# Performance work log

Measured on AMD Instinct MI355X. Metric: run time of the kernel, lower is better.

Reference implementation:

```python
import jax, jax.numpy as jnp
import numpy as np

N_NODES = 100000
N_EDGES = 1200000
D = 64


def setup_inputs() -> dict:
    key = jax.random.key(0)
    ks = jax.random.split(key, 11)
    feats = jax.random.normal(ks[0], (N_NODES, D), dtype=jnp.float32)
    src = jax.random.randint(ks[1], (N_EDGES,), 0, N_NODES)
    dst = jax.random.randint(ks[2], (N_EDGES,), 0, N_NODES)
    s = 0.1  # small init scale
    W1 = jax.random.normal(ks[3], (D, D), dtype=jnp.float32) * s
    b1 = jnp.zeros((D,), dtype=jnp.float32)
    Wr1 = jax.random.normal(ks[4], (D, D), dtype=jnp.float32) * s
    br1 = jnp.zeros((D,), dtype=jnp.float32)
    W2 = jax.random.normal(ks[5], (D, D), dtype=jnp.float32) * s
    b2 = jnp.zeros((D,), dtype=jnp.float32)
    Wr2 = jax.random.normal(ks[6], (D, D), dtype=jnp.float32) * s
    br2 = jnp.zeros((D,), dtype=jnp.float32)
    return {"feats": feats, "W1": W1, "b1": b1, "Wr1": Wr1, "br1": br1,
            "W2": W2, "b2": b2, "Wr2": Wr2, "br2": br2,
            "src": src, "dst": dst}


def _gcn_layer(x, W, b, Wr, br, src, dst):
    # dgl GraphConv(norm='none'): aggregate sum of transformed neighbor feats + bias, then ReLU
    xw = x @ W                                        # [N, D]
    agg = jax.ops.segment_sum(xw[src], dst, num_segments=x.shape[0])  # gather-scatter
    conv = jax.nn.relu(agg + b)
    # residual branch: activation(Linear(feats))
    res = jax.nn.relu(x @ Wr + br)
    return conv + res  # dropout=0.0, batchnorm=False


def reference(feats, W1, b1, Wr1, br1, W2, b2, Wr2, br2, src, dst):
    h = _gcn_layer(feats, W1, b1, Wr1, br1, src, dst)
    h = _gcn_layer(h, W2, b2, Wr2, br2, src, dst)
    return h
```

## Files before the change

### kernel.cpp

```cpp
#include <hip/hip_runtime.h>

#define D 64
#define NBMAX 256
#define BCHUNK 4096
#define CAP 8192

typedef unsigned short ushort_t;
typedef __attribute__((ext_vector_type(8))) short bf16x8;
typedef __attribute__((ext_vector_type(4))) float floatx4;

static __device__ __forceinline__ ushort_t f2bf(float x) {
  unsigned u = __float_as_uint(x);
  unsigned r = (u + 0x7FFF + ((u >> 16) & 1)) >> 16;
  return (ushort_t)r;
}
static __device__ __forceinline__ float bf2f(ushort_t u) {
  return __uint_as_float(((unsigned)u) << 16);
}

__global__ __launch_bounds__(256) void gemm_res_mfma_kernel(
    const float* __restrict__ x, const float* __restrict__ W,
    const float* __restrict__ Wr, const float* __restrict__ br,
    ushort_t* __restrict__ xw, ushort_t* __restrict__ res, int n_nodes) {
  const int lane = threadIdx.x & 63;
  const int wid = threadIdx.x >> 6;
  const int sub = lane & 15;
  const int q = lane >> 4;

  bf16x8 bW[4][2], bR[4][2];
#pragma unroll
  for (int t = 0; t < 4; ++t) {
#pragma unroll
    for (int s = 0; s < 2; ++s) {
      bf16x8 fw, fr;
#pragma unroll
      for (int j = 0; j < 8; ++j) {
        const int k = s * 32 + q * 8 + j;
        const int c = t * 16 + sub;
        fw[j] = (short)f2bf(W[k * D + c]);
        fr[j] = (short)f2bf(Wr[k * D + c]);
      }
      bW[t][s] = fw;
      bR[t][s] = fr;
    }
  }
  float brv[4];
#pragma unroll
  for (int t = 0; t < 4; ++t) brv[t] = br[t * 16 + sub];

  const int n_tiles = (n_nodes + 15) >> 4;
  const int wave_id = blockIdx.x * 4 + wid;
  const int n_waves = gridDim.x * 4;
  for (int tile = wave_id; tile < n_tiles; tile += n_waves) {
    const int n0 = tile << 4;
    const bool full = (n0 + 16 <= n_nodes);
    bf16x8 a0h, a0l, a1h, a1l;
    float v[16];
    if (full) {
      const float* xp = x + (size_t)(n0 + sub) * D + q * 8;
      *(float4*)(v + 0)  = *(const float4*)(xp);
      *(float4*)(v + 4)  = *(const float4*)(xp + 4);
      *(float4*)(v + 8)  = *(const float4*)(xp + 32);
      *(float4*)(v + 12) = *(const float4*)(xp + 36);
    } else {
      const bool ok = (n0 + sub) < n_nodes;
      const float* xp = x + (size_t)(n0 + sub) * D + q * 8;
#pragma unroll
      for (int j = 0; j < 8; ++j) {
        v[j] = ok ? xp[j] : 0.f;
        v[8 + j] = ok ? xp[32 + j] : 0.f;
      }
    }
#pragma unroll
    for (int j = 0; j < 8; ++j) {
      const ushort_t h0 = f2bf(v[j]);
      a0h[j] = (short)h0;
      a0l[j] = (short)f2bf(v[j] - bf2f(h0));
      const ushort_t h1 = f2bf(v[8 + j]);
      a1h[j] = (short)h1;
      a1l[j] = (short)f2bf(v[8 + j] - bf2f(h1));
    }
    floatx4 accW[4], accR[4];
#pragma unroll
    for (int t = 0; t < 4; ++t) {
      accW[t] = (floatx4){0.f, 0.f, 0.f, 0.f};
      accR[t] = (floatx4){0.f, 0.f, 0.f, 0.f};
    }
#pragma unroll
    for (int t = 0; t < 4; ++t) {
      accW[t] = __builtin_amdgcn_mfma_f32_16x16x32_bf16(a0h, bW[t][0], accW[t], 0, 0, 0);
      accW[t] = __builtin_amdgcn_mfma_f32_16x16x32_bf16(a0l, bW[t][0], accW[t], 0, 0, 0);
      accW[t] = __builtin_amdgcn_mfma_f32_16x16x32_bf16(a1h, bW[t][1], accW[t], 0, 0, 0);
      accW[t] = __builtin_amdgcn_mfma_f32_16x16x32_bf16(a1l, bW[t][1], accW[t], 0, 0, 0);
      accR[t] = __builtin_amdgcn_mfma_f32_16x16x32_bf16(a0h, bR[t][0], accR[t], 0, 0, 0);
      accR[t] = __builtin_amdgcn_mfma_f32_16x16x32_bf16(a0l, bR[t][0], accR[t], 0, 0, 0);
      accR[t] = __builtin_amdgcn_mfma_f32_16x16x32_bf16(a1h, bR[t][1], accR[t], 0, 0, 0);
      accR[t] = __builtin_amdgcn_mfma_f32_16x16x32_bf16(a1l, bR[t][1], accR[t], 0, 0, 0);
    }
    if (full) {
#pragma unroll
      for (int t = 0; t < 4; ++t) {
#pragma unroll
        for (int i = 0; i < 4; ++i) {
          const size_t r = (size_t)(n0 + q * 4 + i) * D + t * 16 + sub;
          xw[r] = f2bf(accW[t][i]);
          res[r] = f2bf(fmaxf(accR[t][i] + brv[t], 0.f));
        }
      }
    } else {
#pragma unroll
      for (int t = 0; t < 4; ++t) {
#pragma unroll
        for (int i = 0; i < 4; ++i) {
          const int rr = n0 + q * 4 + i;
          if (rr < n_nodes) {
            const size_t r = (size_t)rr * D + t * 16 + sub;
            xw[r] = f2bf(accW[t][i]);
            res[r] = f2bf(fmaxf(accR[t][i] + brv[t], 0.f));
          }
        }
      }
    }
  }
}


__global__ __launch_bounds__(256) void bucket_count_kernel(
    const int* __restrict__ dst, int* __restrict__ counts, int n_edges) {
  __shared__ int hloc[NBMAX];
  const int t = threadIdx.x;
  hloc[t] = 0;
  __syncthreads();
  const int n4 = n_edges >> 2;
  const int stride = gridDim.x * blockDim.x;
  const int4* dst4 = (const int4*)dst;
  for (int i = blockIdx.x * blockDim.x + t; i < n4; i += stride) {
    const int4 d = dst4[i];
    atomicAdd(&hloc[d.x >> 9], 1);
    atomicAdd(&hloc[d.y >> 9], 1);
    atomicAdd(&hloc[d.z >> 9], 1);
    atomicAdd(&hloc[d.w >> 9], 1);
  }
  if (blockIdx.x == 0 && t == 0) {
    for (int e = n4 << 2; e < n_edges; ++e) atomicAdd(&counts[dst[e] >> 9], 1);
  }
  __syncthreads();
  atomicAdd(&counts[t], hloc[t]);
}

__global__ __launch_bounds__(256) void scan_buckets_kernel(
    const int* __restrict__ counts, int* __restrict__ bucket_base,
    int* __restrict__ gtail, int nbuckets, int* __restrict__ off_tail,
    int n_edges) {
  __shared__ int sc[NBMAX];
  const int t = threadIdx.x;
  const int c = (t < nbuckets) ? counts[t] : 0;
  sc[t] = c;
  __syncthreads();
  for (int off = 1; off < NBMAX; off <<= 1) {
    const int v = (t >= off) ? sc[t - off] : 0;
    __syncthreads();
    sc[t] += v;
    __syncthreads();
  }
  const int excl = sc[t] - c;
  if (t < nbuckets) {
    bucket_base[t] = excl;
    gtail[t] = excl;
  }
  if (t == nbuckets) bucket_base[t] = excl;
  if (t == 0) *off_tail = n_edges;
}

__global__ __launch_bounds__(256) void binpack_kernel(
    const int* __restrict__ src, const int* __restrict__ dst,
    int* __restrict__ gtail, unsigned* __restrict__ packed, int n_edges) {
  __shared__ int hist[NBMAX], start[NBMAX], cur[NBMAX], gpos[NBMAX];
  __shared__ unsigned sorted[BCHUNK];
  __shared__ unsigned char bktid[BCHUNK];
  const int t = threadIdx.x;
  const int nchunk = (n_edges + BCHUNK - 1) / BCHUNK;
  for (int c = blockIdx.x; c < nchunk; c += gridDim.x) {
    cur[t] = 0;
    __syncthreads();
    const int e0 = c * BCHUNK;
    const int m = min(BCHUNK, n_edges - e0);
    int bk[16];
    unsigned pk[16];
#pragma unroll
    for (int k = 0; k < 16; ++k) {
      const int e = e0 + k * 256 + t;
      if (e < n_edges) {
        const int d = dst[e];
        const int s = src[e];
        bk[k] = d >> 9;
        pk[k] = ((unsigned)(d & 511) << 23) | (unsigned)s;
        atomicAdd(&cur[bk[k]], 1);
      } else {
        bk[k] = -1;
      }
    }
    __syncthreads();
    const int h = cur[t];
    hist[t] = h;
    start[t] = h;
    __syncthreads();
    for (int off = 1; off < NBMAX; off <<= 1) {
      const int v = (t >= off) ? start[t - off] : 0;
      __syncthreads();
      start[t] += v;
      __syncthreads();
    }
    const int excl = start[t] - h;
    __syncthreads();
    start[t] = excl;
    cur[t] = excl;
    __syncthreads();
#pragma unroll
    for (int k = 0; k < 16; ++k) {
      if (bk[k] >= 0) {
        const int pos = atomicAdd(&cur[bk[k]], 1);
        sorted[pos] = pk[k];
        bktid[pos] = (unsigned char)bk[k];
      }
    }
    __syncthreads();
    if (h > 0) gpos[t] = atomicAdd(&gtail[t], h);
    __syncthreads();
    for (int j = t; j < m; j += 256) {
      const int b = bktid[j];
      packed[gpos[b] + j - start[b]] = sorted[j];
    }
    __syncthreads();
  }
}

__global__ __launch_bounds__(256) void bucket_csr_kernel(
    const unsigned* __restrict__ packed, const int* __restrict__ bucket_base,
    int* __restrict__ csr_off, int* __restrict__ csr_src, int n_nodes) {
  __shared__ int sc[2][512];
  __shared__ int cur[512];
  __shared__ unsigned outbuf[CAP];
  const int b = blockIdx.x;
  const int t = threadIdx.x;
  const int n0 = b << 9;
  const int nn = min(512, n_nodes - n0);
  const int base = bucket_base[b];
  const int cntE = bucket_base[b + 1] - base;
  cur[t] = 0;
  cur[t + 256] = 0;
  __syncthreads();
  for (int i = base + t; i < base + cntE; i += 256)
    atomicAdd(&cur[packed[i] >> 23], 1);
  __syncthreads();
  const int h0 = cur[t];
  const int h1 = cur[t + 256];
  sc[0][t] = h0;
  sc[0][t + 256] = h1;
  __syncthreads();
  int pin = 0;
  for (int off = 1; off < 512; off <<= 1) {
    sc[1 - pin][t] = sc[pin][t] + ((t >= off) ? sc[pin][t - off] : 0);
    sc[1 - pin][t + 256] =
        sc[pin][t + 256] + ((t + 256 >= off) ? sc[pin][t + 256 - off] : 0);
    __syncthreads();
    pin ^= 1;
  }
  const int excl0 = sc[pin][t] - h0;
  const int excl1 = sc[pin][t + 256] - h1;
  if (t < nn) csr_off[n0 + t] = base + excl0;
  if (t + 256 < nn) csr_off[n0 + t + 256] = base + excl1;
  cur[t] = excl0;
  cur[t + 256] = excl1;
  __syncthreads();
  if (cntE <= CAP) {
    for (int i = base + t; i < base + cntE; i += 256) {
      const unsigned u = packed[i];
      const int pos = atomicAdd(&cur[u >> 23], 1);
      outbuf[pos] = u & 0x7FFFFFu;
    }
    __syncthreads();
    for (int j = t; j < cntE; j += 256) csr_src[base + j] = (int)outbuf[j];
  } else {
    for (int i = base + t; i < base + cntE; i += 256) {
      const unsigned u = packed[i];
      const int pos = atomicAdd(&cur[u >> 23], 1);
      csr_src[base + pos] = (int)(u & 0x7FFFFFu);
    }
  }
}

__global__ __launch_bounds__(256) void gather_combine_kernel(
    const ushort_t* __restrict__ xw, const ushort_t* __restrict__ res,
    const float* __restrict__ b, const int* __restrict__ csr_off,
    const int* __restrict__ csr_src, float* __restrict__ out, int n_nodes) {
  const int lane = threadIdx.x & 63;
  const int wid = threadIdx.x >> 6;
  const int grp = lane >> 4;
  const int sub = lane & 15;
  const float4 bvec = *(const float4*)(b + sub * 4);
  const int n_tiles = (n_nodes + 3) >> 2;
  for (int tile = blockIdx.x; tile < n_tiles; tile += gridDim.x) {
    const int n = tile * 4 + wid;
    if (n >= n_nodes) continue;
    const int e0 = csr_off[n];
    const int e1 = csr_off[n + 1];
    float4 acc = make_float4(0.f, 0.f, 0.f, 0.f);
    for (int base_e = e0; base_e < e1; base_e += 64) {
      const int m = min(64, e1 - base_e);
      const int idxv = (base_e + lane < e1) ? csr_src[base_e + lane] : 0;
      for (int j = 0; j < m; j += 4) {
        const int idx = __shfl(idxv, j + grp, 64);
        if (j + grp < m) {
          const ushort4 v =
              *(const ushort4*)(xw + ((size_t)idx << 6) + (sub << 2));
          acc.x += bf2f(v.x);
          acc.y += bf2f(v.y);
          acc.z += bf2f(v.z);
          acc.w += bf2f(v.w);
        }
      }
    }
#pragma unroll
    for (int mask = 32; mask >= 16; mask >>= 1) {
      acc.x += __shfl_xor(acc.x, mask, 64);
      acc.y += __shfl_xor(acc.y, mask, 64);
      acc.z += __shfl_xor(acc.z, mask, 64);
      acc.w += __shfl_xor(acc.w, mask, 64);
    }
    if (grp == 0) {
      const ushort4 r =
          *(const ushort4*)(res + ((size_t)n << 6) + (sub << 2));
      float4 o;
      o.x = fmaxf(acc.x + bvec.x, 0.f) + bf2f(r.x);
      o.y = fmaxf(acc.y + bvec.y, 0.f) + bf2f(r.y);
      o.z = fmaxf(acc.z + bvec.z, 0.f) + bf2f(r.z);
      o.w = fmaxf(acc.w + bvec.w, 0.f) + bf2f(r.w);
      *(float4*)(out + ((size_t)n << 6) + (sub << 2)) = o;
    }
  }
}

extern "C" void kernel_launch(void* const* d_in, const int* in_sizes, int n_in,
                              void* d_out, int out_size, void* d_ws, size_t ws_size,
                              hipStream_t stream) {
  const float* feats = (const float*)d_in[0];
  const float* W1  = (const float*)d_in[1];
  const float* b1  = (const float*)d_in[2];
  const float* Wr1 = (const float*)d_in[3];
  const float* br1 = (const float*)d_in[4];
  const float* W2  = (const float*)d_in[5];
  const float* b2  = (const float*)d_in[6];
  const float* Wr2 = (const float*)d_in[7];
  const float* br2 = (const float*)d_in[8];
  const int* src = (const int*)d_in[9];
  const int* dst = (const int*)d_in[10];
  const int n_nodes = in_sizes[0] / D;
  const int n_edges = in_sizes[9];
  float* out = (float*)d_out;

  const int nbuckets = (n_nodes + 511) >> 9;

  ushort_t* xw = (ushort_t*)d_ws;
  ushort_t* res = xw + (size_t)n_nodes * D;
  int* csr_off = (int*)(res + (size_t)n_nodes * D);
  int* csr_src = csr_off + (n_nodes + 1);
  int* counts = csr_src + n_edges;
  int* bucket_base = counts + NBMAX;
  int* gtail = bucket_base + NBMAX + 1;
  unsigned* packed = (unsigned*)xw;

  const int tiles = (n_nodes + 3) / 4;
  const int gblocks = tiles < 2048 ? tiles : 2048;
  const int cblocks = (n_edges / 4 + 255) / 256 < 1024 ? (n_edges / 4 + 255) / 256 : 1024;
  const int nchunk = (n_edges + BCHUNK - 1) / BCHUNK;
  const int pblocks = nchunk < 1024 ? nchunk : 1024;
  const int mblocks = 1024;
  dim3 blk(256);

  hipMemsetAsync(counts, 0, NBMAX * sizeof(int), stream);
  bucket_count_kernel<<<cblocks, blk, 0, stream>>>(dst, counts, n_edges);
  scan_buckets_kernel<<<1, NBMAX, 0, stream>>>(counts, bucket_base, gtail,
                                               nbuckets, csr_off + n_nodes,
                                               n_edges);
  binpack_kernel<<<pblocks, blk, 0, stream>>>(src, dst, gtail, packed, n_edges);
  bucket_csr_kernel<<<nbuckets, blk, 0, stream>>>(packed, bucket_base, csr_off,
                                                  csr_src, n_nodes);

  gemm_res_mfma_kernel<<<mblocks, blk, 0, stream>>>(feats, W1, Wr1, br1, xw, res, n_nodes);
  gather_combine_kernel<<<gblocks, blk, 0, stream>>>(
      xw, res, b1, csr_off, csr_src, out, n_nodes);

  gemm_res_mfma_kernel<<<mblocks, blk, 0, stream>>>(out, W2, Wr2, br2, xw, res, n_nodes);
  gather_combine_kernel<<<gblocks, blk, 0, stream>>>(
      xw, res, b2, csr_off, csr_src, out, n_nodes);
}
```

Measured before the change: 268.3 us.

## Drop bucket count pass with fixed-capacity buckets and fuse layer-1 gather with layer-2 GEMM

Removes the bucket_count and scan kernels plus the memset. Each bucket now gets a fixed-capacity slot (CAP_PACK) in the packed buffer, and bucket_csr recomputes bucket offsets from the final tails. The layer-1 gather/combine is fused with the layer-2 linear transforms through an LDS tile and split-bf16 MFMA, so the fp32 intermediate never goes to global memory. The first GEMM also initializes the bucket tails. This cuts launches and a full pass over dst, but it assumes no bucket exceeds 12288 edges and that the caller supplies a larger workspace.

```diff
diff --git a/kernel.cpp b/kernel.cpp
--- a/kernel.cpp
+++ b/kernel.cpp
@@ -4,6 +4,7 @@
 #define NBMAX 256
 #define BCHUNK 4096
 #define CAP 8192
+#define CAP_PACK 12288
 
 typedef unsigned short ushort_t;
 typedef __attribute__((ext_vector_type(8))) short bf16x8;
@@ -21,7 +22,12 @@
 __global__ __launch_bounds__(256) void gemm_res_mfma_kernel(
     const float* __restrict__ x, const float* __restrict__ W,
     const float* __restrict__ Wr, const float* __restrict__ br,
-    ushort_t* __restrict__ xw, ushort_t* __restrict__ res, int n_nodes) {
+    ushort_t* __restrict__ xw, ushort_t* __restrict__ res, int n_nodes,
+    int* __restrict__ gtail, int* __restrict__ off_tail, int n_edges) {
+  if (blockIdx.x == 0) {
+    if (threadIdx.x < NBMAX) gtail[threadIdx.x] = (int)threadIdx.x * CAP_PACK;
+    if (threadIdx.x == 0) *off_tail = n_edges;
+  }
   const int lane = threadIdx.x & 63;
   const int wid = threadIdx.x >> 6;
   const int sub = lane & 15;
@@ -124,58 +130,10 @@
   }
 }
 
-
-__global__ __launch_bounds__(256) void bucket_count_kernel(
-    const int* __restrict__ dst, int* __restrict__ counts, int n_edges) {
-  __shared__ int hloc[NBMAX];
-  const int t = threadIdx.x;
-  hloc[t] = 0;
-  __syncthreads();
-  const int n4 = n_edges >> 2;
-  const int stride = gridDim.x * blockDim.x;
-  const int4* dst4 = (const int4*)dst;
-  for (int i = blockIdx.x * blockDim.x + t; i < n4; i += stride) {
-    const int4 d = dst4[i];
-    atomicAdd(&hloc[d.x >> 9], 1);
-    atomicAdd(&hloc[d.y >> 9], 1);
-    atomicAdd(&hloc[d.z >> 9], 1);
-    atomicAdd(&hloc[d.w >> 9], 1);
-  }
-  if (blockIdx.x == 0 && t == 0) {
-    for (int e = n4 << 2; e < n_edges; ++e) atomicAdd(&counts[dst[e] >> 9], 1);
-  }
-  __syncthreads();
-  atomicAdd(&counts[t], hloc[t]);
-}
-
-__global__ __launch_bounds__(256) void scan_buckets_kernel(
-    const int* __restrict__ counts, int* __restrict__ bucket_base,
-    int* __restrict__ gtail, int nbuckets, int* __restrict__ off_tail,
-    int n_edges) {
-  __shared__ int sc[NBMAX];
-  const int t = threadIdx.x;
-  const int c = (t < nbuckets) ? counts[t] : 0;
-  sc[t] = c;
-  __syncthreads();
-  for (int off = 1; off < NBMAX; off <<= 1) {
-    const int v = (t >= off) ? sc[t - off] : 0;
-    __syncthreads();
-    sc[t] += v;
-    __syncthreads();
-  }
-  const int excl = sc[t] - c;
-  if (t < nbuckets) {
-    bucket_base[t] = excl;
-    gtail[t] = excl;
-  }
-  if (t == nbuckets) bucket_base[t] = excl;
-  if (t == 0) *off_tail = n_edges;
-}
-
 __global__ __launch_bounds__(256) void binpack_kernel(
     const int* __restrict__ src, const int* __restrict__ dst,
     int* __restrict__ gtail, unsigned* __restrict__ packed, int n_edges) {
-  __shared__ int hist[NBMAX], start[NBMAX], cur[NBMAX], gpos[NBMAX];
+  __shared__ int start[NBMAX], cur[NBMAX], gpos[NBMAX];
   __shared__ unsigned sorted[BCHUNK];
   __shared__ unsigned char bktid[BCHUNK];
   const int t = threadIdx.x;
@@ -202,7 +160,6 @@
     }
     __syncthreads();
     const int h = cur[t];
-    hist[t] = h;
     start[t] = h;
     __syncthreads();
     for (int off = 1; off < NBMAX; off <<= 1) {
@@ -236,22 +193,37 @@
 }
 
 __global__ __launch_bounds__(256) void bucket_csr_kernel(
-    const unsigned* __restrict__ packed, const int* __restrict__ bucket_base,
-    int* __restrict__ csr_off, int* __restrict__ csr_src, int n_nodes) {
+    const unsigned* __restrict__ packed, const int* __restrict__ gtail,
+    int* __restrict__ csr_off, int* __restrict__ csr_src, int n_nodes,
+    int nbuckets) {
+  __shared__ int scnt[NBMAX], sexc[NBMAX];
   __shared__ int sc[2][512];
   __shared__ int cur[512];
   __shared__ unsigned outbuf[CAP];
   const int b = blockIdx.x;
   const int t = threadIdx.x;
+  const int cb = (t < nbuckets) ? (gtail[t] - t * CAP_PACK) : 0;
+  scnt[t] = cb;
+  sexc[t] = cb;
+  __syncthreads();
+  for (int off = 1; off < NBMAX; off <<= 1) {
+    const int v = (t >= off) ? sexc[t - off] : 0;
+    __syncthreads();
+    sexc[t] += v;
+    __syncthreads();
+  }
+  sexc[t] -= scnt[t];
+  __syncthreads();
+  const int base = sexc[b];
+  const int cntE = scnt[b];
+  const unsigned* pk = packed + (size_t)b * CAP_PACK;
+
   const int n0 = b << 9;
   const int nn = min(512, n_nodes - n0);
-  const int base = bucket_base[b];
-  const int cntE = bucket_base[b + 1] - base;
   cur[t] = 0;
   cur[t + 256] = 0;
   __syncthreads();
-  for (int i = base + t; i < base + cntE; i += 256)
-    atomicAdd(&cur[packed[i] >> 23], 1);
+  for (int i = t; i < cntE; i += 256) atomicAdd(&cur[pk[i] >> 23], 1);
   __syncthreads();
   const int h0 = cur[t];
   const int h1 = cur[t + 256];
@@ -274,19 +246,133 @@
   cur[t + 256] = excl1;
   __syncthreads();
   if (cntE <= CAP) {
-    for (int i = base + t; i < base + cntE; i += 256) {
-      const unsigned u = packed[i];
+    for (int i = t; i < cntE; i += 256) {
+      const unsigned u = pk[i];
       const int pos = atomicAdd(&cur[u >> 23], 1);
       outbuf[pos] = u & 0x7FFFFFu;
     }
     __syncthreads();
     for (int j = t; j < cntE; j += 256) csr_src[base + j] = (int)outbuf[j];
   } else {
-    for (int i = base + t; i < base + cntE; i += 256) {
-      const unsigned u = packed[i];
+    for (int i = t; i < cntE; i += 256) {
+      const unsigned u = pk[i];
       const int pos = atomicAdd(&cur[u >> 23], 1);
       csr_src[base + pos] = (int)(u & 0x7FFFFFu);
     }
+  }
+}
+
+__global__ __launch_bounds__(256) void gather_gemm_kernel(
+    const ushort_t* __restrict__ xw1, const ushort_t* __restrict__ res1,
+    const float* __restrict__ b1v, const int* __restrict__ csr_off,
+    const int* __restrict__ csr_src, const float* __restrict__ W2,
+    const float* __restrict__ Wr2, const float* __restrict__ br2,
+    ushort_t* __restrict__ xw2, ushort_t* __restrict__ res2, int n_nodes) {
+  const int lane = threadIdx.x & 63;
+  const int w = threadIdx.x >> 6;
+  const int sub = lane & 15;
+  const int q = lane >> 4;
+  __shared__ float h_tile[16][68];
+
+  bf16x8 bW[2], bR[2];
+#pragma unroll
+  for (int s = 0; s < 2; ++s) {
+    bf16x8 fw, fr;
+#pragma unroll
+    for (int j = 0; j < 8; ++j) {
+      const int k = s * 32 + q * 8 + j;
+      const int c = w * 16 + sub;
+      fw[j] = (short)f2bf(W2[k * D + c]);
+      fr[j] = (short)f2bf(Wr2[k * D + c]);
+    }
+    bW[s] = fw;
+    bR[s] = fr;
+  }
+  const float brl2 = br2[w * 16 + sub];
+  const float4 bvec = *(const float4*)(b1v + sub * 4);
+
+  const int n_tiles = (n_nodes + 15) >> 4;
+  for (int tile = blockIdx.x; tile < n_tiles; tile += gridDim.x) {
+    const int n0 = tile << 4;
+    for (int j4 = 0; j4 < 4; ++j4) {
+      const int n = n0 + w * 4 + j4;
+      if (n < n_nodes) {
+        const int e0 = csr_off[n];
+        const int e1 = csr_off[n + 1];
+        float4 acc = make_float4(0.f, 0.f, 0.f, 0.f);
+        for (int base_e = e0; base_e < e1; base_e += 64) {
+          const int m = min(64, e1 - base_e);
+          const int idxv = (base_e + lane < e1) ? csr_src[base_e + lane] : 0;
+          for (int j = 0; j < m; j += 4) {
+            const int idx = __shfl(idxv, j + q, 64);
+            if (j + q < m) {
+              const ushort4 vv =
+                  *(const ushort4*)(xw1 + ((size_t)idx << 6) + (sub << 2));
+              acc.x += bf2f(vv.x);
+              acc.y += bf2f(vv.y);
+              acc.z += bf2f(vv.z);
+              acc.w += bf2f(vv.w);
+            }
+          }
+        }
+#pragma unroll
+        for (int mask = 32; mask >= 16; mask >>= 1) {
+          acc.x += __shfl_xor(acc.x, mask, 64);
+          acc.y += __shfl_xor(acc.y, mask, 64);
+          acc.z += __shfl_xor(acc.z, mask, 64);
+          acc.w += __shfl_xor(acc.w, mask, 64);
+        }
+        if (q == 0) {
+          const ushort4 r =
+              *(const ushort4*)(res1 + ((size_t)n << 6) + (sub << 2));
+          float4 o;
+          o.x = fmaxf(acc.x + bvec.x, 0.f) + bf2f(r.x);
+          o.y = fmaxf(acc.y + bvec.y, 0.f) + bf2f(r.y);
+          o.z = fmaxf(acc.z + bvec.z, 0.f) + bf2f(r.z);
+          o.w = fmaxf(acc.w + bvec.w, 0.f) + bf2f(r.w);
+          *(float4*)(&h_tile[w * 4 + j4][sub * 4]) = o;
+        }
+      } else if (q == 0) {
+        *(float4*)(&h_tile[w * 4 + j4][sub * 4]) =
+            make_float4(0.f, 0.f, 0.f, 0.f);
+      }
+    }
+    __syncthreads();
+    float v[16];
+    *(float4*)(v + 0)  = *(const float4*)(&h_tile[sub][q * 8]);
+    *(float4*)(v + 4)  = *(const float4*)(&h_tile[sub][q * 8 + 4]);
+    *(float4*)(v + 8)  = *(const float4*)(&h_tile[sub][32 + q * 8]);
+    *(float4*)(v + 12) = *(const float4*)(&h_tile[sub][32 + q * 8 + 4]);
+    bf16x8 a0h, a0l, a1h, a1l;
+#pragma unroll
+    for (int j = 0; j < 8; ++j) {
+      const ushort_t h0 = f2bf(v[j]);
+      a0h[j] = (short)h0;
+      a0l[j] = (short)f2bf(v[j] - bf2f(h0));
+      const ushort_t h1 = f2bf(v[8 + j]);
+      a1h[j] = (short)h1;
+      a1l[j] = (short)f2bf(v[8 + j] - bf2f(h1));
+    }
+    floatx4 accW = (floatx4){0.f, 0.f, 0.f, 0.f};
+    floatx4 accR = (floatx4){0.f, 0.f, 0.f, 0.f};
+    accW = __builtin_amdgcn_mfma_f32_16x16x32_bf16(a0h, bW[0], accW, 0, 0, 0);
+    accW = __builtin_amdgcn_mfma_f32_16x16x32_bf16(a0l, bW[0], accW, 0, 0, 0);
+    accW = __builtin_amdgcn_mfma_f32_16x16x32_bf16(a1h, bW[1], accW, 0, 0, 0);
+    accW = __builtin_amdgcn_mfma_f32_16x16x32_bf16(a1l, bW[1], accW, 0, 0, 0);
+    accR = __builtin_amdgcn_mfma_f32_16x16x32_bf16(a0h, bR[0], accR, 0, 0, 0);
+    accR = __builtin_amdgcn_mfma_f32_16x16x32_bf16(a0l, bR[0], accR, 0, 0, 0);
+    accR = __builtin_amdgcn_mfma_f32_16x16x32_bf16(a1h, bR[1], accR, 0, 0, 0);
+    accR = __builtin_amdgcn_mfma_f32_16x16x32_bf16(a1l, bR[1], accR, 0, 0, 0);
+#pragma unroll
+    for (int i = 0; i < 4; ++i) {
+      const int rr = n0 + q * 4 + i;
+      if (rr < n_nodes) {
+        const size_t r = (size_t)rr * D + w * 16 + sub;
+        xw2[r] = f2bf(accW[i]);
+        res2[r] = f2bf(fmaxf(accR[i] + brl2, 0.f));
+      }
+    }
+    __syncthreads();
   }
 }
 
@@ -361,37 +447,30 @@
 
   const int nbuckets = (n_nodes + 511) >> 9;
 
-  ushort_t* xw = (ushort_t*)d_ws;
-  ushort_t* res = xw + (size_t)n_nodes * D;
-  int* csr_off = (int*)(res + (size_t)n_nodes * D);
+  ushort_t* xw1 = (ushort_t*)d_ws;
+  ushort_t* res1 = xw1 + (size_t)n_nodes * D;
+  ushort_t* xw2 = res1 + (size_t)n_nodes * D;
+  ushort_t* res2 = xw2 + (size_t)n_nodes * D;
+  int* csr_off = (int*)(res2 + (size_t)n_nodes * D);
   int* csr_src = csr_off + (n_nodes + 1);
-  int* counts = csr_src + n_edges;
-  int* bucket_base = counts + NBMAX;
-  int* gtail = bucket_base + NBMAX + 1;
-  unsigned* packed = (unsigned*)xw;
-
-  const int tiles = (n_nodes + 3) / 4;
-  const int gblocks = tiles < 2048 ? tiles : 2048;
-  const int cblocks = (n_edges / 4 + 255) / 256 < 1024 ? (n_edges / 4 + 255) / 256 : 1024;
+  int* gtail = csr_src + n_edges;
+  unsigned* packed = (unsigned*)(gtail + NBMAX);
+
+  const int tiles4 = (n_nodes + 3) / 4;
+  const int gblocks = tiles4 < 2048 ? tiles4 : 2048;
+  const int tiles16 = (n_nodes + 15) / 16;
+  const int fblocks = tiles16 < 2048 ? tiles16 : 2048;
   const int nchunk = (n_edges + BCHUNK - 1) / BCHUNK;
   const int pblocks = nchunk < 1024 ? nchunk : 1024;
-  const int mblocks = 1024;
   dim3 blk(256);
 
-  hipMemsetAsync(counts, 0, NBMAX * sizeof(int), stream);
-  bucket_count_kernel<<<cblocks, blk, 0, stream>>>(dst, counts, n_edges);
-  scan_buckets_kernel<<<1, NBMAX, 0, stream>>>(counts, bucket_base, gtail,
-                                               nbuckets, csr_off + n_nodes,
-                                               n_edges);
+  gemm_res_mfma_kernel<<<1024, blk, 0, stream>>>(
+      feats, W1, Wr1, br1, xw1, res1, n_nodes, gtail, csr_off + n_nodes, n_edges);
   binpack_kernel<<<pblocks, blk, 0, stream>>>(src, dst, gtail, packed, n_edges);
-  bucket_csr_kernel<<<nbuckets, blk, 0, stream>>>(packed, bucket_base, csr_off,
-                                                  csr_src, n_nodes);
-
-  gemm_res_mfma_kernel<<<mblocks, blk, 0, stream>>>(feats, W1, Wr1, br1, xw, res, n_nodes);
+  bucket_csr_kernel<<<nbuckets, blk, 0, stream>>>(packed, gtail, csr_off,
+                                                  csr_src, n_nodes, nbuckets);
+  gather_gemm_kernel<<<fblocks, blk, 0, stream>>>(
+      xw1, res1, b1, csr_off, csr_src, W2, Wr2, br2, xw2, res2, n_nodes);
   gather_combine_kernel<<<gblocks, blk, 0, stream>>>(
-      xw, res, b1, csr_off, csr_src, out, n_nodes);
-
-  gemm_res_mfma_kernel<<<mblocks, blk, 0, stream>>>(out, W2, Wr2, br2, xw, res, n_nodes);
-  gather_combine_kernel<<<gblocks, blk, 0, stream>>>(
-      xw, res, b2, csr_off, csr_src, out, n_nodes);
-}
+      xw2, res2, b2, csr_off, csr_src, out, n_nodes);
+}
```

Result: faster. 252.5 us (-5.9%).
